# Performance work log

Measured on AMD Instinct MI355X. Metric: run time of the kernel, lower is better.

Reference implementation:

```python
import jax, jax.numpy as jnp
from jax import lax
import numpy as np

D_MODEL = 1024
D_STATE = 16
D_CONV = 4
EXPAND = 2
D_INNER = EXPAND * D_MODEL  # 2048
DT_RANK = D_MODEL // 16     # 64
BATCH = 2
SEQLEN = 1024


def setup_inputs() -> dict:
    key = jax.random.key(0)
    ks = iter(jax.random.split(key, 32))

    def nrm(shape, s=0.02):
        return jax.random.normal(next(ks), shape, jnp.float32) * s

    def mamba_params():
        return dict(
            Win=nrm((2 * D_INNER, D_MODEL)), bin=jnp.zeros((2 * D_INNER,), jnp.float32),
            convw=nrm((D_INNER, D_CONV), 0.1), convb=jnp.zeros((D_INNER,), jnp.float32),
            Wx=nrm((DT_RANK + 2 * D_STATE, D_INNER)),
            Wdt=nrm((D_INNER, DT_RANK), 0.1), bdt=nrm((D_INNER,), 0.1),
            Alog=jnp.log(jnp.broadcast_to(jnp.arange(1, D_STATE + 1, dtype=jnp.float32), (D_INNER, D_STATE))),
            Dsk=jnp.ones((D_INNER,), jnp.float32),
            Wout=nrm((D_MODEL, D_INNER)), bout=jnp.zeros((D_MODEL,), jnp.float32),
        )

    inp = {"x": jax.random.normal(next(ks), (BATCH, SEQLEN, D_MODEL), jnp.float32)}
    for pref, p in (("f_", mamba_params()), ("b_", mamba_params())):
        for k, v in p.items():
            inp[pref + k] = v
    inp["proj_W"] = nrm((D_MODEL, 2 * D_MODEL))
    inp["proj_b"] = jnp.zeros((D_MODEL,), jnp.float32)
    return inp


def selective_scan(u, delta, A, Bm, Cm, Dsk):
    # u, delta: (B,L,Di); Bm, Cm: (B,L,N); A: (Di,N); Dsk: (Di,)
    def step(h, inp):
        u_t, d_t, b_t, c_t = inp  # (B,Di),(B,Di),(B,N),(B,N)
        dA = jnp.exp(d_t[..., None] * A)                      # (B,Di,N)
        h = h * dA + (d_t * u_t)[..., None] * b_t[:, None, :]  # (B,Di,N)
        y = jnp.einsum('bdn,bn->bd', h, c_t)
        return h, y

    h0 = jnp.zeros((u.shape[0], A.shape[0], A.shape[1]), u.dtype)
    xs = (u.transpose(1, 0, 2), delta.transpose(1, 0, 2),
          Bm.transpose(1, 0, 2), Cm.transpose(1, 0, 2))
    _, ys = lax.scan(step, h0, xs)
    return ys.transpose(1, 0, 2) + u * Dsk  # (B,L,Di)


def mamba_fwd(x, Win, bin_, convw, convb, Wx, Wdt, bdt, Alog, Dsk, Wout, bout):
    xz = x @ Win.T + bin_                      # (B,L,2*Di)
    xin, z = jnp.split(xz, 2, axis=-1)
    # causal depthwise conv over time: (B,Di,L)
    xc = lax.conv_general_dilated(
        xin.transpose(0, 2, 1), convw[:, None, :], (1,), [(D_CONV - 1, 0)],
        dimension_numbers=('NCH', 'OIH', 'NCH'), feature_group_count=D_INNER)
    u = jax.nn.silu(xc.transpose(0, 2, 1) + convb)  # (B,L,Di)
    xdbl = u @ Wx.T                                 # (B,L,dt_rank+2N)
    dt, Bm, Cm = jnp.split(xdbl, [DT_RANK, DT_RANK + D_STATE], axis=-1)
    delta = jax.nn.softplus(dt @ Wdt.T + bdt)       # (B,L,Di)
    A = -jnp.exp(Alog)
    y = selective_scan(u, delta, A, Bm, Cm, Dsk)
    y = y * jax.nn.silu(z)
    return y @ Wout.T + bout


def reference(x,
              f_Win, f_bin, f_convw, f_convb, f_Wx, f_Wdt, f_bdt, f_Alog, f_Dsk, f_Wout, f_bout,
              b_Win, b_bin, b_convw, b_convb, b_Wx, b_Wdt, b_bdt, b_Alog, b_Dsk, b_Wout, b_bout,
              proj_W, proj_b):
    out_f = mamba_fwd(x, f_Win, f_bin, f_convw, f_convb, f_Wx, f_Wdt, f_bdt, f_Alog, f_Dsk, f_Wout, f_bout)
    xr = jnp.flip(x, axis=1)
    out_b = mamba_fwd(xr, b_Win, b_bin, b_convw, b_convb, b_Wx, b_Wdt, b_bdt, b_Alog, b_Dsk, b_Wout, b_bout)
    out_b = jnp.flip(out_b, axis=1)
    out = jnp.concatenate([out_f, out_b], axis=-1)  # (B,L,2*d_model)
    return out @ proj_W.T + proj_b
```

## Files before the change

kernel.cpp:

```cpp
#include <hip/hip_runtime.h>
#include <math.h>

#define D_MODEL 1024
#define D_STATE 16
#define D_CONV  4
#define D_INNER 2048
#define DT_RANK 64
#define BATCH   2
#define SEQLEN  1024
#define MROWS   2048
#define XDBL_LD 128
#define NCHUNK  32
#define CLEN    (SEQLEN / NCHUNK)
#define NCHG    8192

typedef __attribute__((ext_vector_type(8))) short bf16x8;
typedef __attribute__((ext_vector_type(4))) float f32x4;

#define BARR() asm volatile("s_barrier" ::: "memory")
#define VMW(n) asm volatile("s_waitcnt vmcnt(" #n ")" ::: "memory")

static __device__ __forceinline__ float sigmoidf_(float x) {
    return 1.f / (1.f + __expf(-x));
}
static __device__ __forceinline__ unsigned short bf16rn(float f) {
    unsigned u = __float_as_uint(f);
    return (unsigned short)((u + 0x7FFFu + ((u >> 16) & 1u)) >> 16);
}
static __device__ __forceinline__ void hl_split(float f, unsigned short& h, unsigned short& l) {
    h = bf16rn(f);
    l = bf16rn(f - __uint_as_float((unsigned)h << 16));
}
static __device__ __forceinline__ float us2f(unsigned short u) {
    return __uint_as_float((unsigned)u << 16);
}

static __device__ __forceinline__
void split_block(const float* __restrict__ in, int R, int C, int ldin,
                 unsigned short* __restrict__ out, int Rout, bool flip,
                 int blk, int tid)
{
    int q = blk * 256 + tid;
    int qpr = C >> 2;
    int row = q / qpr;
    int c4 = (q - row * qpr) << 2;
    if (row >= Rout) return;
    unsigned short h[4] = {0, 0, 0, 0}, l[4] = {0, 0, 0, 0};
    if (row < R) {
        int sr = row;
        if (flip) { int b = row >> 10, t = row & 1023; sr = (b << 10) + (1023 - t); }
        float4 v = *(const float4*)(in + (size_t)sr * ldin + c4);
        float f[4] = {v.x, v.y, v.z, v.w};
        #pragma unroll
        for (int i = 0; i < 4; ++i) hl_split(f[i], h[i], l[i]);
    }
    size_t ob = (size_t)row * (2 * C);
    *(ushort4*)(out + ob + c4)     = make_ushort4(h[0], h[1], h[2], h[3]);
    *(ushort4*)(out + ob + C + c4) = make_ushort4(l[0], l[1], l[2], l[3]);
}

__global__ __launch_bounds__(256)
void prep1_kernel(const float* __restrict__ x,
                  const float* __restrict__ Win0, const float* __restrict__ Win1,
                  const float* __restrict__ Wx0,  const float* __restrict__ Wx1,
                  const float* __restrict__ Wdt0, const float* __restrict__ Wdt1,
                  unsigned short* xc0, unsigned short* xc1,
                  unsigned short* Winb0, unsigned short* Winb1,
                  unsigned short* Wxb0, unsigned short* Wxb1,
                  unsigned short* Wdtb0, unsigned short* Wdtb1)
{
    int b = blockIdx.x, tid = threadIdx.x;
    if      (b < 2048)  split_block(x,    MROWS, D_MODEL, D_MODEL, xc0,  MROWS, false, b,        tid);
    else if (b < 4096)  split_block(x,    MROWS, D_MODEL, D_MODEL, xc1,  MROWS, true,  b - 2048, tid);
    else if (b < 8192)  split_block(Win0, 4096,  D_MODEL, D_MODEL, Winb0, 4096, false, b - 4096, tid);
    else if (b < 12288) split_block(Win1, 4096,  D_MODEL, D_MODEL, Winb1, 4096, false, b - 8192, tid);
    else if (b < 12544) split_block(Wx0,  96,    D_INNER, D_INNER, Wxb0,  128,  false, b - 12288, tid);
    else if (b < 12800) split_block(Wx1,  96,    D_INNER, D_INNER, Wxb1,  128,  false, b - 12544, tid);
    else if (b < 12928) split_block(Wdt0, D_INNER, DT_RANK, DT_RANK, Wdtb0, D_INNER, false, b - 12800, tid);
    else                split_block(Wdt1, D_INNER, DT_RANK, DT_RANK, Wdtb1, D_INNER, false, b - 12928, tid);
}

__global__ __launch_bounds__(256)
void prep2_kernel(const float* __restrict__ Wout0, const float* __restrict__ Wout1,
                  unsigned short* Woutb0, unsigned short* Woutb1)
{
    int b = blockIdx.x, tid = threadIdx.x;
    if (b < 2048) split_block(Wout0, D_MODEL, D_INNER, D_INNER, Woutb0, D_MODEL, false, b, tid);
    else          split_block(Wout1, D_MODEL, D_INNER, D_INNER, Woutb1, D_MODEL, false, b - 2048, tid);
}

#define SWZ(row) (((row) >> 1) & 3)
#define RDA(p, kk, row) (*(const bf16x8*)&AS[p][kk][row][(fs ^ SWZ(row)) << 3])
#define RDB(p, kk, row) (*(const bf16x8*)&BS[p][kk][row][(fs ^ SWZ(row)) << 3])

#define KTILE(MODE, kt) do { \
    const int p_ = (kt) & 1; \
    bf16x8 bF[4]; \
    {  \
        bf16x8 aF[4]; \
        _Pragma("unroll") for (int f = 0; f < 4; ++f) { int rw = wm + f * 16 + fr; aF[f] = RDA(p_, 0, rw); } \
        _Pragma("unroll") for (int g = 0; g < 4; ++g) { int rw = wn + g * 16 + fr; bF[g] = RDB(p_, 0, rw); } \
        if (MODE < 2) stageA((kt) + 1, 1); \
        BARR(); __builtin_amdgcn_s_setprio(1); \
        _Pragma("unroll") for (int f = 0; f < 4; ++f) \
        _Pragma("unroll") for (int g = 0; g < 4; ++g) \
            acc[f][g] = __builtin_amdgcn_mfma_f32_16x16x32_bf16(aF[f], bF[g], acc[f][g], 0, 0, 0); \
        __builtin_amdgcn_s_setprio(0); BARR(); \
    } \
    {  \
        if (MODE == 2) { VMW(0); } else { VMW(8); } \
        bf16x8 aF[4]; \
        _Pragma("unroll") for (int f = 0; f < 4; ++f) { int rw = wm + 64 + f * 16 + fr; aF[f] = RDA(p_, 0, rw); } \
        if (MODE == 0) stageB((kt) + 2, 0); \
        BARR(); __builtin_amdgcn_s_setprio(1); \
        _Pragma("unroll") for (int f = 0; f < 4; ++f) \
        _Pragma("unroll") for (int g = 0; g < 4; ++g) \
            acc[4 + f][g] = __builtin_amdgcn_mfma_f32_16x16x32_bf16(aF[f], bF[g], acc[4 + f][g], 0, 0, 0); \
        __builtin_amdgcn_s_setprio(0); BARR(); \
    } \
    {  \
        bf16x8 aF[4]; \
        _Pragma("unroll") for (int f = 0; f < 4; ++f) { int rw = wm + f * 16 + fr; aF[f] = RDA(p_, 1, rw); } \
        _Pragma("unroll") for (int g = 0; g < 4; ++g) { int rw = wn + g * 16 + fr; bF[g] = RDB(p_, 1, rw); } \
        if (MODE == 0) stageA((kt) + 2, 0); \
        BARR(); __builtin_amdgcn_s_setprio(1); \
        _Pragma("unroll") for (int f = 0; f < 4; ++f) \
        _Pragma("unroll") for (int g = 0; g < 4; ++g) \
            acc[f][g] = __builtin_amdgcn_mfma_f32_16x16x32_bf16(aF[f], bF[g], acc[f][g], 0, 0, 0); \
        __builtin_amdgcn_s_setprio(0); BARR(); \
    } \
    {  \
        if (MODE == 0) { VMW(8); } else if (MODE == 1) { VMW(4); } \
        bf16x8 aF[4]; \
        _Pragma("unroll") for (int f = 0; f < 4; ++f) { int rw = wm + 64 + f * 16 + fr; aF[f] = RDA(p_, 1, rw); } \
        if (MODE == 0) stageB((kt) + 2, 1); \
        BARR(); __builtin_amdgcn_s_setprio(1); \
        _Pragma("unroll") for (int f = 0; f < 4; ++f) \
        _Pragma("unroll") for (int g = 0; g < 4; ++g) \
            acc[4 + f][g] = __builtin_amdgcn_mfma_f32_16x16x32_bf16(aF[f], bF[g], acc[4 + f][g], 0, 0, 0); \
        __builtin_amdgcn_s_setprio(0); BARR(); \
    } \
} while (0)

template<int ACT, bool PART>
__global__ __launch_bounds__(512, 1)
void gemm256(const unsigned short* __restrict__ A0,
             const unsigned short* __restrict__ A1,
             const unsigned short* __restrict__ W0,
             const unsigned short* __restrict__ W1,
             const float* __restrict__ bias0,
             const float* __restrict__ bias1,
             float* __restrict__ C0, float* __restrict__ C1,
             float* __restrict__ part,
             int ldc, int N, int K, int nks, int KTS)
{
    __shared__ unsigned short AS[2][2][256][32];
    __shared__ unsigned short BS[2][2][256][32];

    const int tid = threadIdx.x;
    const int lane = tid & 63;
    const int wid = tid >> 6;

    const int z = blockIdx.z;
    const int dir = z / nks;
    const int ks = z - dir * nks;
    const unsigned short* A = dir ? A1 : A0;
    const unsigned short* W = dir ? W1 : W0;

    const int nbx = gridDim.x;
    const int nwg = nbx * gridDim.y;
    int bid = blockIdx.y * nbx + blockIdx.x;
    int q8 = nwg >> 3;
    int swz = (bid & 7) * q8 + (bid >> 3);
    const int bm = (swz / nbx) * 256;
    const int bn = (swz % nbx) * 256;

    const int ldg = 2 * K;
    const int Kc = KTS * 64;
    const int kbase = ks * Kc;
    const int NT = 3 * KTS;

    const int wm = (wid >> 2) * 128;
    const int wn = (wid & 3) * 64;
    const int fr = lane & 15;
    const int fs = lane >> 4;

    f32x4 acc[8][4];
    #pragma unroll
    for (int i = 0; i < 8; ++i)
        #pragma unroll
        for (int j = 0; j < 4; ++j) {
            f32x4 zv = {0.f, 0.f, 0.f, 0.f};
            acc[i][j] = zv;
        }

    auto koffA = [&](int t) { int sg = t / KTS; int w = t - sg * KTS;
                              return ((sg == 1) ? K : 0) + kbase + w * 64; };
    auto koffB = [&](int t) { int sg = t / KTS; int w = t - sg * KTS;
                              return ((sg == 2) ? K : 0) + kbase + w * 64; };

    auto stageA = [&](int t, int kk) {
        int ko = koffA(t) + kk * 32;
        unsigned short* dst = &AS[t & 1][kk][0][0];
        #pragma unroll
        for (int i = 0; i < 2; ++i) {
            int s = i * 512 + tid;
            int row = s >> 2, sl = s & 3, lsl = sl ^ SWZ(row);
            const unsigned short* src = A + (size_t)(bm + row) * ldg + ko + lsl * 8;
            __builtin_amdgcn_global_load_lds(
                (const __attribute__((address_space(1))) void*)src,
                (__attribute__((address_space(3))) void*)(dst + s * 8), 16, 0, 0);
        }
    };
    auto stageB = [&](int t, int kk) {
        int ko = koffB(t) + kk * 32;
        unsigned short* dst = &BS[t & 1][kk][0][0];
        #pragma unroll
        for (int i = 0; i < 2; ++i) {
            int s = i * 512 + tid;
            int row = s >> 2, sl = s & 3, lsl = sl ^ SWZ(row);
            const unsigned short* src = W + (size_t)(bn + row) * ldg + ko + lsl * 8;
            __builtin_amdgcn_global_load_lds(
                (const __attribute__((address_space(1))) void*)src,
                (__attribute__((address_space(3))) void*)(dst + s * 8), 16, 0, 0);
        }
    };

    stageB(0, 0); stageA(0, 0); stageB(0, 1); stageA(0, 1);
    stageB(1, 0); stageA(1, 0); stageB(1, 1);
    VMW(6);
    BARR();

    for (int kt = 0; kt < NT - 2; ++kt) KTILE(0, kt);
    KTILE(1, NT - 2);
    KTILE(2, NT - 1);

    if (PART) {
        float* P = part + (size_t)z * ((size_t)MROWS * N);
        #pragma unroll
        for (int i = 0; i < 8; ++i)
            #pragma unroll
            for (int j = 0; j < 4; ++j) {
                int coln = bn + wn + j * 16 + fr;
                #pragma unroll
                for (int r = 0; r < 4; ++r) {
                    int rowm = bm + wm + i * 16 + fs * 4 + r;
                    P[(size_t)rowm * N + coln] = acc[i][j][r];
                }
            }
    } else {
        const float* bias = dir ? bias1 : bias0;
        float* C = dir ? C1 : C0;
        #pragma unroll
        for (int i = 0; i < 8; ++i)
            #pragma unroll
            for (int j = 0; j < 4; ++j) {
                int coln = bn + wn + j * 16 + fr;
                float bv = bias ? bias[coln] : 0.f;
                #pragma unroll
                for (int r = 0; r < 4; ++r) {
                    int rowm = bm + wm + i * 16 + fs * 4 + r;
                    float v = acc[i][j][r] + bv;
                    if (ACT == 1) v = (v > 20.f) ? v : log1pf(__expf(v));
                    C[(size_t)rowm * ldc + coln] = v;
                }
            }
    }
}

template<int ACT, bool PART>
__global__ __launch_bounds__(256)
void gemm_mfma(const unsigned short* __restrict__ A0,
               const unsigned short* __restrict__ A1,
               const unsigned short* __restrict__ W0,
               const unsigned short* __restrict__ W1,
               const float* __restrict__ bias0,
               const float* __restrict__ bias1,
               float* __restrict__ C0, float* __restrict__ C1,
               float* __restrict__ part,
               int ldc, int N, int K, int nks)
{
    __shared__ __align__(16) unsigned short As[128 * 32];
    __shared__ __align__(16) unsigned short Bs[128 * 32];

    const int tid = threadIdx.x;
    const int lane = tid & 63;
    const int wid = tid >> 6;

    const int z = blockIdx.z;
    const int dir = z / nks;
    const int ks = z - dir * nks;
    const unsigned short* A = dir ? A1 : A0;
    const unsigned short* W = dir ? W1 : W0;

    const int nbx = gridDim.x;
    const int nwg = nbx * gridDim.y;
    int bid = blockIdx.y * nbx + blockIdx.x;
    int q8 = nwg >> 3;
    int swz = (nwg >= 8) ? (bid & 7) * q8 + (bid >> 3) : bid;
    const int bm = (swz / nbx) * 128;
    const int bn = (swz % nbx) * 128;

    const int ldg = 2 * K;
    const int Kc = K / nks;
    const int kbase = ks * Kc;

    f32x4 acc[4][4];
    #pragma unroll
    for (int i = 0; i < 4; ++i)
        #pragma unroll
        for (int j = 0; j < 4; ++j) {
            f32x4 zv = {0.f, 0.f, 0.f, 0.f};
            acc[i][j] = zv;
        }

    const int r0 = tid >> 2;
    const int k0s = (tid & 3) ^ ((r0 >> 1) & 3);
    const int r1 = (256 + tid) >> 2;
    const int k1s = (tid & 3) ^ ((r1 >> 1) & 3);

    unsigned short* As_w0 = &As[(wid << 6) * 8];
    unsigned short* As_w1 = &As[(256 + (wid << 6)) * 8];
    unsigned short* Bs_w0 = &Bs[(wid << 6) * 8];
    unsigned short* Bs_w1 = &Bs[(256 + (wid << 6)) * 8];

    const int wm = (wid >> 1) * 64;
    const int wn = (wid & 1) * 64;
    const int fr = lane & 15;
    const int fs = lane >> 4;

    const int KS = Kc >> 5;
    #pragma unroll 1
    for (int seg = 0; seg < 3; ++seg) {
        const int aoff = ((seg == 1) ? K : 0) + kbase;
        const int boff = ((seg == 2) ? K : 0) + kbase;
        #pragma unroll 1
        for (int kt = 0; kt < KS; ++kt) {
            const int kk = kt << 5;
            const unsigned short* ga0 = A + (size_t)(bm + r0) * ldg + aoff + kk + k0s * 8;
            const unsigned short* ga1 = A + (size_t)(bm + r1) * ldg + aoff + kk + k1s * 8;
            const unsigned short* gw0 = W + (size_t)(bn + r0) * ldg + boff + kk + k0s * 8;
            const unsigned short* gw1 = W + (size_t)(bn + r1) * ldg + boff + kk + k1s * 8;
            __builtin_amdgcn_global_load_lds(
                (const __attribute__((address_space(1))) void*)ga0,
                (__attribute__((address_space(3))) void*)As_w0, 16, 0, 0);
            __builtin_amdgcn_global_load_lds(
                (const __attribute__((address_space(1))) void*)ga1,
                (__attribute__((address_space(3))) void*)As_w1, 16, 0, 0);
            __builtin_amdgcn_global_load_lds(
                (const __attribute__((address_space(1))) void*)gw0,
                (__attribute__((address_space(3))) void*)Bs_w0, 16, 0, 0);
            __builtin_amdgcn_global_load_lds(
                (const __attribute__((address_space(1))) void*)gw1,
                (__attribute__((address_space(3))) void*)Bs_w1, 16, 0, 0);
            __syncthreads();

            bf16x8 aF[4], bF[4];
            #pragma unroll
            for (int f = 0; f < 4; ++f) {
                int ra = wm + f * 16 + fr;
                int sa = fs ^ ((ra >> 1) & 3);
                aF[f] = *(const bf16x8*)&As[ra * 32 + sa * 8];
                int rb = wn + f * 16 + fr;
                int sb = fs ^ ((rb >> 1) & 3);
                bF[f] = *(const bf16x8*)&Bs[rb * 32 + sb * 8];
            }
            #pragma unroll
            for (int i = 0; i < 4; ++i)
                #pragma unroll
                for (int j = 0; j < 4; ++j)
                    acc[i][j] = __builtin_amdgcn_mfma_f32_16x16x32_bf16(
                        aF[i], bF[j], acc[i][j], 0, 0, 0);
            __syncthreads();
        }
    }

    if (PART) {
        float* P = part + (size_t)z * ((size_t)MROWS * N);
        #pragma unroll
        for (int i = 0; i < 4; ++i)
            #pragma unroll
            for (int j = 0; j < 4; ++j) {
                int coln = bn + wn + j * 16 + fr;
                #pragma unroll
                for (int r = 0; r < 4; ++r) {
                    int rowm = bm + wm + i * 16 + fs * 4 + r;
                    P[(size_t)rowm * N + coln] = acc[i][j][r];
                }
            }
    } else {
        const float* bias = dir ? bias1 : bias0;
        float* C = dir ? C1 : C0;
        #pragma unroll
        for (int i = 0; i < 4; ++i)
            #pragma unroll
            for (int j = 0; j < 4; ++j) {
                int coln = bn + wn + j * 16 + fr;
                float bv = bias ? bias[coln] : 0.f;
                #pragma unroll
                for (int r = 0; r < 4; ++r) {
                    int rowm = bm + wm + i * 16 + fs * 4 + r;
                    float v = acc[i][j][r] + bv;
                    if (ACT == 1) v = (v > 20.f) ? v : log1pf(__expf(v));
                    C[(size_t)rowm * ldc + coln] = v;
                }
            }
    }
}

__global__ __launch_bounds__(256)
void reduce_xdbl_k(const float* __restrict__ part,
                   float* __restrict__ xdbl0, float* __restrict__ xdbl1,
                   unsigned short* __restrict__ dtb0, unsigned short* __restrict__ dtb1)
{
    const int dz = blockIdx.z;
    const float* P = part + (size_t)dz * 16 * MROWS * XDBL_LD;
    float* xdbl = dz ? xdbl1 : xdbl0;
    unsigned short* dtb = dz ? dtb1 : dtb0;
    int i = blockIdx.x * 256 + threadIdx.x;
    int row = i >> 5;
    int c4 = (i & 31) << 2;
    float4 s = make_float4(0.f, 0.f, 0.f, 0.f);
    #pragma unroll
    for (int k = 0; k < 16; ++k) {
        float4 v = *(const float4*)(P + (size_t)k * MROWS * XDBL_LD + (size_t)row * XDBL_LD + c4);
        s.x += v.x; s.y += v.y; s.z += v.z; s.w += v.w;
    }
    *(float4*)(xdbl + (size_t)row * XDBL_LD + c4) = s;
    if (c4 < DT_RANK) {
        float f[4] = {s.x, s.y, s.z, s.w};
        unsigned short h[4], l[4];
        #pragma unroll
        for (int j = 0; j < 4; ++j) hl_split(f[j], h[j], l[j]);
        *(ushort4*)(dtb + (size_t)row * (2 * DT_RANK) + c4) = make_ushort4(h[0], h[1], h[2], h[3]);
        *(ushort4*)(dtb + (size_t)row * (2 * DT_RANK) + DT_RANK + c4) = make_ushort4(l[0], l[1], l[2], l[3]);
    }
}

__global__ __launch_bounds__(256)
void mid_kernel(const float* __restrict__ part2,
                const float* __restrict__ bout0, const float* __restrict__ bout1,
                unsigned short* __restrict__ tmpb,
                const float* __restrict__ projW, unsigned short* __restrict__ pWb)
{
    const int dz = blockIdx.z;
    const int tid = threadIdx.x;
    if (dz == 2) {
        split_block(projW, D_MODEL, 2 * D_MODEL, 2 * D_MODEL, pWb, D_MODEL, false, blockIdx.x, tid);
        return;
    }
    const float* P = part2 + (size_t)dz * 4 * MROWS * D_MODEL;
    const float* bias = dz ? bout1 : bout0;
    const int colofs = dz ? D_MODEL : 0;
    int i = blockIdx.x * 256 + tid;
    int row = i >> 8;
    int c4 = (i & 255) << 2;
    float4 s = make_float4(bias[c4], bias[c4 + 1], bias[c4 + 2], bias[c4 + 3]);
    #pragma unroll
    for (int k = 0; k < 4; ++k) {
        float4 v = *(const float4*)(P + (size_t)k * MROWS * D_MODEL + (size_t)row * D_MODEL + c4);
        s.x += v.x; s.y += v.y; s.z += v.z; s.w += v.w;
    }
    int orow = row;
    if (dz) { int bb = row >> 10, t = row & 1023; orow = (bb << 10) + 1023 - t; }
    float f[4] = {s.x, s.y, s.z, s.w};
    unsigned short h[4], l[4];
    #pragma unroll
    for (int j = 0; j < 4; ++j) hl_split(f[j], h[j], l[j]);
    *(ushort4*)(tmpb + (size_t)orow * 4096 + colofs + c4) = make_ushort4(h[0], h[1], h[2], h[3]);
    *(ushort4*)(tmpb + (size_t)orow * 4096 + 2048 + colofs + c4) = make_ushort4(l[0], l[1], l[2], l[3]);
}

__global__ __launch_bounds__(256)
void reduce_out_k(const float* __restrict__ part, const float* __restrict__ bias,
                  float* __restrict__ out)
{
    int i = blockIdx.x * 256 + threadIdx.x;
    int row = i >> 8;
    int c4 = (i & 255) << 2;
    float4 s = make_float4(bias[c4], bias[c4 + 1], bias[c4 + 2], bias[c4 + 3]);
    #pragma unroll
    for (int k = 0; k < 8; ++k) {
        float4 v = *(const float4*)(part + (size_t)k * MROWS * D_MODEL + (size_t)row * D_MODEL + c4);
        s.x += v.x; s.y += v.y; s.z += v.z; s.w += v.w;
    }
    *(float4*)(out + (size_t)row * D_MODEL + c4) = s;
}

__global__ __launch_bounds__(256)
void conv_silu_kernel(const float* __restrict__ xz0, const float* __restrict__ xz1,
                      const float* __restrict__ cw0, const float* __restrict__ cw1,
                      const float* __restrict__ cb0, const float* __restrict__ cb1,
                      unsigned short* __restrict__ ub0, unsigned short* __restrict__ ub1)
{
    const int dz = blockIdx.z;
    const float* xz = dz ? xz1 : xz0;
    const float* convw = dz ? cw1 : cw0;
    const float* convb = dz ? cb1 : cb0;
    unsigned short* ub = dz ? ub1 : ub0;
    int idx = blockIdx.x * 256 + threadIdx.x;
    int d = idx % D_INNER;
    int r = idx / D_INNER;
    int t = r % SEQLEN;
    float acc = convb[d];
    #pragma unroll
    for (int k = 0; k < D_CONV; ++k) {
        int back = D_CONV - 1 - k;
        if (t - back >= 0)
            acc += xz[(size_t)(r - back) * (2 * D_INNER) + d] * convw[d * D_CONV + k];
    }
    float v = acc * sigmoidf_(acc);
    unsigned short h, l;
    hl_split(v, h, l);
    ub[(size_t)r * (2 * D_INNER) + d] = h;
    ub[(size_t)r * (2 * D_INNER) + D_INNER + d] = l;
}

__global__ __launch_bounds__(256)
void scan_phase1(const float* __restrict__ delta0, const float* __restrict__ delta1,
                 const unsigned short* __restrict__ ub0, const unsigned short* __restrict__ ub1,
                 const float* __restrict__ xdbl0, const float* __restrict__ xdbl1,
                 const float* __restrict__ Alog0, const float* __restrict__ Alog1,
                 float* __restrict__ aprod, float* __restrict__ hfin)
{
    const int gid = blockIdx.x * 256 + threadIdx.x;
    const int chg = gid & (NCHG - 1);
    const int chunk = gid >> 13;
    const int dir = chg >> 12;
    const int bd = chg & 4095;
    const int b = bd >> 11, d = bd & 2047;
    const float* delta = dir ? delta1 : delta0;
    const unsigned short* ub = dir ? ub1 : ub0;
    const float* xdbl = dir ? xdbl1 : xdbl0;
    const float* Alog = dir ? Alog1 : Alog0;

    float Av[16], h[16], ap[16];
    #pragma unroll
    for (int n = 0; n < 16; ++n) {
        Av[n] = -__expf(Alog[d * D_STATE + n]);
        h[n] = 0.f; ap[n] = 1.f;
    }
    const int t0 = chunk * CLEN;
    for (int t = t0; t < t0 + CLEN; ++t) {
        const size_t r = (size_t)b * SEQLEN + t;
        float dlt = delta[r * D_INNER + d];
        float uu = us2f(ub[r * 4096 + d]) + us2f(ub[r * 4096 + 2048 + d]);
        float du = dlt * uu;
        float4 bq[4];
        #pragma unroll
        for (int q = 0; q < 4; ++q)
            bq[q] = *(const float4*)(xdbl + r * XDBL_LD + DT_RANK + q * 4);
        #pragma unroll
        for (int n = 0; n < 16; ++n) {
            float Bv = ((const float*)&bq[n >> 2])[n & 3];
            float dA = __expf(dlt * Av[n]);
            h[n] = h[n] * dA + du * Bv;
            ap[n] *= dA;
        }
    }
    float* pa = aprod + (size_t)chunk * (NCHG * 16) + (size_t)chg * 16;
    float* pf = hfin  + (size_t)chunk * (NCHG * 16) + (size_t)chg * 16;
    #pragma unroll
    for (int q = 0; q < 4; ++q) {
        *(float4*)(pa + q * 4) = make_float4(ap[q*4], ap[q*4+1], ap[q*4+2], ap[q*4+3]);
        *(float4*)(pf + q * 4) = make_float4(h[q*4], h[q*4+1], h[q*4+2], h[q*4+3]);
    }
}

__global__ __launch_bounds__(256)
void scan_phase2(float* __restrict__ aprod ,
                 const float* __restrict__ hfin)
{
    const int gid = blockIdx.x * 256 + threadIdx.x;
    float h = 0.f;
    for (int c = 0; c < NCHUNK; ++c) {
        const size_t idx = (size_t)c * (NCHG * 16) + gid;
        float a = aprod[idx];
        float f = hfin[idx];
        aprod[idx] = h;
        h = a * h + f;
    }
}

__global__ __launch_bounds__(256)
void scan_phase3(const float* __restrict__ delta0, const float* __restrict__ delta1,
                 unsigned short* __restrict__ ub0, unsigned short* __restrict__ ub1,
                 const float* __restrict__ xdbl0, const float* __restrict__ xdbl1,
                 const float* __restrict__ Alog0, const float* __restrict__ Alog1,
                 const float* __restrict__ Dsk0, const float* __restrict__ Dsk1,
                 const float* __restrict__ xz0, const float* __restrict__ xz1,
                 const float* __restrict__ hin)
{
    const int gid = blockIdx.x * 256 + threadIdx.x;
    const int chg = gid & (NCHG - 1);
    const int chunk = gid >> 13;
    const int dir = chg >> 12;
    const int bd = chg & 4095;
    const int b = bd >> 11, d = bd & 2047;
    const float* delta = dir ? delta1 : delta0;
    unsigned short* ub = dir ? ub1 : ub0;
    const float* xdbl = dir ? xdbl1 : xdbl0;
    const float* Alog = dir ? Alog1 : Alog0;
    const float* Dsk = dir ? Dsk1 : Dsk0;
    const float* xz = dir ? xz1 : xz0;

    float Av[16], h[16];
    const float* ph = hin + (size_t)chunk * (NCHG * 16) + (size_t)chg * 16;
    #pragma unroll
    for (int n = 0; n < 16; ++n) {
        Av[n] = -__expf(Alog[d * D_STATE + n]);
        h[n] = ph[n];
    }
    const float Dv = Dsk[d];
    const int t0 = chunk * CLEN;
    for (int t = t0; t < t0 + CLEN; ++t) {
        const size_t r = (size_t)b * SEQLEN + t;
        float dlt = delta[r * D_INNER + d];
        float uu = us2f(ub[r * 4096 + d]) + us2f(ub[r * 4096 + 2048 + d]);
        float du = dlt * uu;
        float4 bq[4], cq[4];
        #pragma unroll
        for (int q = 0; q < 4; ++q) {
            bq[q] = *(const float4*)(xdbl + r * XDBL_LD + DT_RANK + q * 4);
            cq[q] = *(const float4*)(xdbl + r * XDBL_LD + DT_RANK + D_STATE + q * 4);
        }
        float p0 = 0.f, p1 = 0.f, p2 = 0.f, p3 = 0.f;
        #pragma unroll
        for (int n = 0; n < 16; ++n) {
            float Bv = ((const float*)&bq[n >> 2])[n & 3];
            float Cv = ((const float*)&cq[n >> 2])[n & 3];
            float dA = __expf(dlt * Av[n]);
            h[n] = h[n] * dA + du * Bv;
            if ((n & 3) == 0) p0 += h[n] * Cv;
            else if ((n & 3) == 1) p1 += h[n] * Cv;
            else if ((n & 3) == 2) p2 += h[n] * Cv;
            else p3 += h[n] * Cv;
        }
        float y = ((p0 + p1) + (p2 + p3)) + uu * Dv;
        float zv = xz[r * (2 * D_INNER) + D_INNER + d];
        float v = y * (zv * sigmoidf_(zv));
        unsigned short hh, ll;
        hl_split(v, hh, ll);
        ub[r * 4096 + d] = hh;
        ub[r * 4096 + 2048 + d] = ll;
    }
}

extern "C" void kernel_launch(void* const* d_in, const int* in_sizes, int n_in,
                              void* d_out, int out_size, void* d_ws, size_t ws_size,
                              hipStream_t stream)
{
    const float* x = (const float*)d_in[0];
    const float* proj_W = (const float*)d_in[23];
    const float* proj_b = (const float*)d_in[24];
    float* out = (float*)d_out;

    const float *Win[2], *bin_[2], *convw[2], *convb[2], *Wx[2], *Wdt[2], *bdt[2],
                *Alog[2], *Dsk[2], *Wout[2], *bout[2];
    for (int dir = 0; dir < 2; ++dir) {
        const int base = 1 + dir * 11;
        Win[dir]   = (const float*)d_in[base + 0];
        bin_[dir]  = (const float*)d_in[base + 1];
        convw[dir] = (const float*)d_in[base + 2];
        convb[dir] = (const float*)d_in[base + 3];
        Wx[dir]    = (const float*)d_in[base + 4];
        Wdt[dir]   = (const float*)d_in[base + 5];
        bdt[dir]   = (const float*)d_in[base + 6];
        Alog[dir]  = (const float*)d_in[base + 7];
        Dsk[dir]   = (const float*)d_in[base + 8];
        Wout[dir]  = (const float*)d_in[base + 9];
        bout[dir]  = (const float*)d_in[base + 10];
    }

    char* ws = (char*)d_ws;
    const size_t MB = 1ull << 20;
    float* xz[2]            = {(float*)(ws + 0 * MB),   (float*)(ws + 32 * MB)};
    unsigned short* ub[2]   = {(unsigned short*)(ws + 64 * MB),
                               (unsigned short*)(ws + 80 * MB)};
    unsigned short* Winb[2] = {(unsigned short*)(ws + 96 * MB),
                               (unsigned short*)(ws + 112 * MB)};
    unsigned short* xc[2]   = {(unsigned short*)(ws + 128 * MB),
                               (unsigned short*)(ws + 136 * MB)};
    float* part             = (float*)(ws + 112 * MB);
    float* part2            = (float*)(ws + 0 * MB);
    float* delta[2]         = {(float*)(ws + 112 * MB), (float*)(ws + 128 * MB)};
    unsigned short* Woutb[2]= {(unsigned short*)(ws + 96 * MB),
                               (unsigned short*)(ws + 104 * MB)};
    unsigned short* yzb[2]  = {ub[0], ub[1]};
    unsigned short* tmpb    = ub[0];
    unsigned short* pWb     = ub[1];
    unsigned short* Wxb[2]  = {(unsigned short*)(ws + 144 * MB), (unsigned short*)(ws + 145 * MB)};
    unsigned short* Wdtb[2] = {(unsigned short*)(ws + 146 * MB), (unsigned short*)(ws + 146 * MB + 512 * 1024)};
    unsigned short* dtb[2]  = {(unsigned short*)(ws + 147 * MB), (unsigned short*)(ws + 147 * MB + 512 * 1024)};
    float* xdbl[2]          = {(float*)(ws + 148 * MB), (float*)(ws + 149 * MB)};
    float* aprod            = (float*)(ws + 150 * MB);
    float* hfin             = (float*)(ws + 167 * MB);

    dim3 blk(256);

    prep1_kernel<<<13056, blk, 0, stream>>>(
        x, Win[0], Win[1], Wx[0], Wx[1], Wdt[0], Wdt[1],
        xc[0], xc[1], Winb[0], Winb[1], Wxb[0], Wxb[1], Wdtb[0], Wdtb[1]);

    gemm256<0, false><<<dim3(16, 8, 2), dim3(512), 0, stream>>>(
        xc[0], xc[1], Winb[0], Winb[1], bin_[0], bin_[1], xz[0], xz[1],
        nullptr, 4096, 4096, D_MODEL, 1, 16);

    prep2_kernel<<<4096, blk, 0, stream>>>(Wout[0], Wout[1], Woutb[0], Woutb[1]);

    conv_silu_kernel<<<dim3((MROWS * D_INNER) / 256, 1, 2), blk, 0, stream>>>(
        xz[0], xz[1], convw[0], convw[1], convb[0], convb[1], ub[0], ub[1]);

    gemm_mfma<0, true><<<dim3(1, 16, 32), blk, 0, stream>>>(
        ub[0], ub[1], Wxb[0], Wxb[1], nullptr, nullptr, nullptr, nullptr,
        part, XDBL_LD, XDBL_LD, D_INNER, 16);

    reduce_xdbl_k<<<dim3(256, 1, 2), blk, 0, stream>>>(
        part, xdbl[0], xdbl[1], dtb[0], dtb[1]);

    gemm_mfma<1, false><<<dim3(16, 16, 2), blk, 0, stream>>>(
        dtb[0], dtb[1], Wdtb[0], Wdtb[1], bdt[0], bdt[1], delta[0], delta[1],
        nullptr, D_INNER, D_INNER, DT_RANK, 1);

    scan_phase1<<<NCHUNK * NCHG / 256, blk, 0, stream>>>(
        delta[0], delta[1], ub[0], ub[1], xdbl[0], xdbl[1], Alog[0], Alog[1],
        aprod, hfin);
    scan_phase2<<<NCHG * 16 / 256, blk, 0, stream>>>(aprod, hfin);
    scan_phase3<<<NCHUNK * NCHG / 256, blk, 0, stream>>>(
        delta[0], delta[1], ub[0], ub[1], xdbl[0], xdbl[1], Alog[0], Alog[1],
        Dsk[0], Dsk[1], xz[0], xz[1], aprod);

    gemm256<0, true><<<dim3(4, 8, 8), dim3(512), 0, stream>>>(
        yzb[0], yzb[1], Woutb[0], Woutb[1], nullptr, nullptr, nullptr, nullptr,
        part2, D_MODEL, D_MODEL, D_INNER, 4, 8);

    mid_kernel<<<dim3(2048, 1, 3), blk, 0, stream>>>(
        part2, bout[0], bout[1], tmpb, proj_W, pWb);

    gemm256<0, true><<<dim3(4, 8, 8), dim3(512), 0, stream>>>(
        tmpb, nullptr, pWb, nullptr, nullptr, nullptr, nullptr, nullptr,
        part2, D_MODEL, D_MODEL, 2 * D_MODEL, 8, 4);

    reduce_out_k<<<2048, blk, 0, stream>>>(part2, proj_b, out);
}
```

Before: 491.4 us.

## Share unflipped input across directions and fold Wout split into conv kernel

The in-projection GEMM now runs once over the unflipped bf16-split input with the two directions' weights concatenated along N. The backward half flips rows at store time, which removes the separate flipped copy of x and its split pass. The Wout hi/lo split moves from its own kernel into an extra grid slice of the conv/SiLU kernel, saving a launch. KTS becomes a template parameter so the k-offset division is resolved at compile time, and the main K loop is marked not to unroll. The risk is scattered row writes in the flipped epilogue and a heavier combined conv kernel.

After: 482.3 us. No clear change (-1.9%).

```diff
diff --git a/kernel.cpp b/kernel.cpp
--- a/kernel.cpp
+++ b/kernel.cpp
@@ -64,29 +64,19 @@
                   const float* __restrict__ Win0, const float* __restrict__ Win1,
                   const float* __restrict__ Wx0,  const float* __restrict__ Wx1,
                   const float* __restrict__ Wdt0, const float* __restrict__ Wdt1,
-                  unsigned short* xc0, unsigned short* xc1,
+                  unsigned short* xc0,
                   unsigned short* Winb0, unsigned short* Winb1,
                   unsigned short* Wxb0, unsigned short* Wxb1,
                   unsigned short* Wdtb0, unsigned short* Wdtb1)
 {
     int b = blockIdx.x, tid = threadIdx.x;
     if      (b < 2048)  split_block(x,    MROWS, D_MODEL, D_MODEL, xc0,  MROWS, false, b,        tid);
-    else if (b < 4096)  split_block(x,    MROWS, D_MODEL, D_MODEL, xc1,  MROWS, true,  b - 2048, tid);
-    else if (b < 8192)  split_block(Win0, 4096,  D_MODEL, D_MODEL, Winb0, 4096, false, b - 4096, tid);
-    else if (b < 12288) split_block(Win1, 4096,  D_MODEL, D_MODEL, Winb1, 4096, false, b - 8192, tid);
-    else if (b < 12544) split_block(Wx0,  96,    D_INNER, D_INNER, Wxb0,  128,  false, b - 12288, tid);
-    else if (b < 12800) split_block(Wx1,  96,    D_INNER, D_INNER, Wxb1,  128,  false, b - 12544, tid);
-    else if (b < 12928) split_block(Wdt0, D_INNER, DT_RANK, DT_RANK, Wdtb0, D_INNER, false, b - 12800, tid);
-    else                split_block(Wdt1, D_INNER, DT_RANK, DT_RANK, Wdtb1, D_INNER, false, b - 12928, tid);
-}
-
-__global__ __launch_bounds__(256)
-void prep2_kernel(const float* __restrict__ Wout0, const float* __restrict__ Wout1,
-                  unsigned short* Woutb0, unsigned short* Woutb1)
-{
-    int b = blockIdx.x, tid = threadIdx.x;
-    if (b < 2048) split_block(Wout0, D_MODEL, D_INNER, D_INNER, Woutb0, D_MODEL, false, b, tid);
-    else          split_block(Wout1, D_MODEL, D_INNER, D_INNER, Woutb1, D_MODEL, false, b - 2048, tid);
+    else if (b < 6144)  split_block(Win0, 4096,  D_MODEL, D_MODEL, Winb0, 4096, false, b - 2048, tid);
+    else if (b < 10240) split_block(Win1, 4096,  D_MODEL, D_MODEL, Winb1, 4096, false, b - 6144, tid);
+    else if (b < 10496) split_block(Wx0,  96,    D_INNER, D_INNER, Wxb0,  128,  false, b - 10240, tid);
+    else if (b < 10752) split_block(Wx1,  96,    D_INNER, D_INNER, Wxb1,  128,  false, b - 10496, tid);
+    else if (b < 10880) split_block(Wdt0, D_INNER, DT_RANK, DT_RANK, Wdtb0, D_INNER, false, b - 10752, tid);
+    else                split_block(Wdt1, D_INNER, DT_RANK, DT_RANK, Wdtb1, D_INNER, false, b - 10880, tid);
 }
 
 #define SWZ(row) (((row) >> 1) & 3)
@@ -142,7 +132,7 @@
     } \
 } while (0)
 
-template<int ACT, bool PART>
+template<int ACT, bool PART, int KTS, bool DUALN>
 __global__ __launch_bounds__(512, 1)
 void gemm256(const unsigned short* __restrict__ A0,
              const unsigned short* __restrict__ A1,
@@ -152,7 +142,7 @@
              const float* __restrict__ bias1,
              float* __restrict__ C0, float* __restrict__ C1,
              float* __restrict__ part,
-             int ldc, int N, int K, int nks, int KTS)
+             int ldc, int N, int K, int nks)
 {
     __shared__ unsigned short AS[2][2][256][32];
     __shared__ unsigned short BS[2][2][256][32];
@@ -162,10 +152,8 @@
     const int wid = tid >> 6;
 
     const int z = blockIdx.z;
-    const int dir = z / nks;
-    const int ks = z - dir * nks;
-    const unsigned short* A = dir ? A1 : A0;
-    const unsigned short* W = dir ? W1 : W0;
+    const int zdir = z / nks;
+    const int ks = z - zdir * nks;
 
     const int nbx = gridDim.x;
     const int nwg = nbx * gridDim.y;
@@ -175,10 +163,16 @@
     const int bm = (swz / nbx) * 256;
     const int bn = (swz % nbx) * 256;
 
+    int dn, bnn;
+    if (DUALN) { dn = (bn >= (N >> 1)) ? 1 : 0; bnn = bn - dn * (N >> 1); }
+    else       { dn = zdir; bnn = bn; }
+    const unsigned short* A = (DUALN || dn == 0) ? A0 : A1;
+    const unsigned short* W = dn ? W1 : W0;
+
     const int ldg = 2 * K;
+    constexpr int NT = 3 * KTS;
     const int Kc = KTS * 64;
     const int kbase = ks * Kc;
-    const int NT = 3 * KTS;
 
     const int wm = (wid >> 2) * 128;
     const int wn = (wid & 3) * 64;
@@ -194,10 +188,12 @@
             acc[i][j] = zv;
         }
 
-    auto koffA = [&](int t) { int sg = t / KTS; int w = t - sg * KTS;
-                              return ((sg == 1) ? K : 0) + kbase + w * 64; };
-    auto koffB = [&](int t) { int sg = t / KTS; int w = t - sg * KTS;
-                              return ((sg == 2) ? K : 0) + kbase + w * 64; };
+    auto koffA = [&](int t) { unsigned tu = (unsigned)t; unsigned sg = tu / KTS;
+                              unsigned w = tu - sg * KTS;
+                              return (int)((sg == 1 ? (unsigned)K : 0u) + kbase + w * 64); };
+    auto koffB = [&](int t) { unsigned tu = (unsigned)t; unsigned sg = tu / KTS;
+                              unsigned w = tu - sg * KTS;
+                              return (int)((sg == 2 ? (unsigned)K : 0u) + kbase + w * 64); };
 
     auto stageA = [&](int t, int kk) {
         int ko = koffA(t) + kk * 32;
@@ -219,7 +215,7 @@
         for (int i = 0; i < 2; ++i) {
             int s = i * 512 + tid;
             int row = s >> 2, sl = s & 3, lsl = sl ^ SWZ(row);
-            const unsigned short* src = W + (size_t)(bn + row) * ldg + ko + lsl * 8;
+            const unsigned short* src = W + (size_t)(bnn + row) * ldg + ko + lsl * 8;
             __builtin_amdgcn_global_load_lds(
                 (const __attribute__((address_space(1))) void*)src,
                 (__attribute__((address_space(3))) void*)(dst + s * 8), 16, 0, 0);
@@ -231,6 +227,7 @@
     VMW(6);
     BARR();
 
+    #pragma unroll 1
     for (int kt = 0; kt < NT - 2; ++kt) KTILE(0, kt);
     KTILE(1, NT - 2);
     KTILE(2, NT - 1);
@@ -241,7 +238,7 @@
         for (int i = 0; i < 8; ++i)
             #pragma unroll
             for (int j = 0; j < 4; ++j) {
-                int coln = bn + wn + j * 16 + fr;
+                int coln = bnn + wn + j * 16 + fr;
                 #pragma unroll
                 for (int r = 0; r < 4; ++r) {
                     int rowm = bm + wm + i * 16 + fs * 4 + r;
@@ -249,20 +246,22 @@
                 }
             }
     } else {
-        const float* bias = dir ? bias1 : bias0;
-        float* C = dir ? C1 : C0;
+        const float* bias = dn ? bias1 : bias0;
+        float* C = dn ? C1 : C0;
         #pragma unroll
         for (int i = 0; i < 8; ++i)
             #pragma unroll
             for (int j = 0; j < 4; ++j) {
-                int coln = bn + wn + j * 16 + fr;
+                int coln = bnn + wn + j * 16 + fr;
                 float bv = bias ? bias[coln] : 0.f;
                 #pragma unroll
                 for (int r = 0; r < 4; ++r) {
                     int rowm = bm + wm + i * 16 + fs * 4 + r;
                     float v = acc[i][j][r] + bv;
                     if (ACT == 1) v = (v > 20.f) ? v : log1pf(__expf(v));
-                    C[(size_t)rowm * ldc + coln] = v;
+                    int crow = rowm;
+                    if (DUALN && dn) { int bb = rowm >> 10, t = rowm & 1023; crow = (bb << 10) + 1023 - t; }
+                    C[(size_t)crow * ldc + coln] = v;
                 }
             }
     }
@@ -488,17 +487,26 @@
 }
 
 __global__ __launch_bounds__(256)
-void conv_silu_kernel(const float* __restrict__ xz0, const float* __restrict__ xz1,
+void conv_prep_kernel(const float* __restrict__ xz0, const float* __restrict__ xz1,
                       const float* __restrict__ cw0, const float* __restrict__ cw1,
                       const float* __restrict__ cb0, const float* __restrict__ cb1,
-                      unsigned short* __restrict__ ub0, unsigned short* __restrict__ ub1)
+                      unsigned short* __restrict__ ub0, unsigned short* __restrict__ ub1,
+                      const float* __restrict__ Wout0, const float* __restrict__ Wout1,
+                      unsigned short* __restrict__ Woutb0, unsigned short* __restrict__ Woutb1)
 {
     const int dz = blockIdx.z;
+    const int tid = threadIdx.x;
+    if (dz == 2) {
+        int b = blockIdx.x;
+        if (b < 2048) split_block(Wout0, D_MODEL, D_INNER, D_INNER, Woutb0, D_MODEL, false, b, tid);
+        else if (b < 4096) split_block(Wout1, D_MODEL, D_INNER, D_INNER, Woutb1, D_MODEL, false, b - 2048, tid);
+        return;
+    }
     const float* xz = dz ? xz1 : xz0;
     const float* convw = dz ? cw1 : cw0;
     const float* convb = dz ? cb1 : cb0;
     unsigned short* ub = dz ? ub1 : ub0;
-    int idx = blockIdx.x * 256 + threadIdx.x;
+    int idx = blockIdx.x * 256 + tid;
     int d = idx % D_INNER;
     int r = idx / D_INNER;
     int t = r % SEQLEN;
@@ -679,8 +687,7 @@
                                (unsigned short*)(ws + 80 * MB)};
     unsigned short* Winb[2] = {(unsigned short*)(ws + 96 * MB),
                                (unsigned short*)(ws + 112 * MB)};
-    unsigned short* xc[2]   = {(unsigned short*)(ws + 128 * MB),
-                               (unsigned short*)(ws + 136 * MB)};
+    unsigned short* xc0     = (unsigned short*)(ws + 128 * MB);
     float* part             = (float*)(ws + 112 * MB);
     float* part2            = (float*)(ws + 0 * MB);
     float* delta[2]         = {(float*)(ws + 112 * MB), (float*)(ws + 128 * MB)};
@@ -698,18 +705,17 @@
 
     dim3 blk(256);
 
-    prep1_kernel<<<13056, blk, 0, stream>>>(
+    prep1_kernel<<<11008, blk, 0, stream>>>(
         x, Win[0], Win[1], Wx[0], Wx[1], Wdt[0], Wdt[1],
-        xc[0], xc[1], Winb[0], Winb[1], Wxb[0], Wxb[1], Wdtb[0], Wdtb[1]);
-
-    gemm256<0, false><<<dim3(16, 8, 2), dim3(512), 0, stream>>>(
-        xc[0], xc[1], Winb[0], Winb[1], bin_[0], bin_[1], xz[0], xz[1],
-        nullptr, 4096, 4096, D_MODEL, 1, 16);
-
-    prep2_kernel<<<4096, blk, 0, stream>>>(Wout[0], Wout[1], Woutb[0], Woutb[1]);
-
-    conv_silu_kernel<<<dim3((MROWS * D_INNER) / 256, 1, 2), blk, 0, stream>>>(
-        xz[0], xz[1], convw[0], convw[1], convb[0], convb[1], ub[0], ub[1]);
+        xc0, Winb[0], Winb[1], Wxb[0], Wxb[1], Wdtb[0], Wdtb[1]);
+
+    gemm256<0, false, 16, true><<<dim3(32, 8, 1), dim3(512), 0, stream>>>(
+        xc0, nullptr, Winb[0], Winb[1], bin_[0], bin_[1], xz[0], xz[1],
+        nullptr, 4096, 8192, D_MODEL, 1);
+
+    conv_prep_kernel<<<dim3((MROWS * D_INNER) / 256, 1, 3), blk, 0, stream>>>(
+        xz[0], xz[1], convw[0], convw[1], convb[0], convb[1], ub[0], ub[1],
+        Wout[0], Wout[1], Woutb[0], Woutb[1]);
 
     gemm_mfma<0, true><<<dim3(1, 16, 32), blk, 0, stream>>>(
         ub[0], ub[1], Wxb[0], Wxb[1], nullptr, nullptr, nullptr, nullptr,
@@ -730,16 +736,16 @@
         delta[0], delta[1], ub[0], ub[1], xdbl[0], xdbl[1], Alog[0], Alog[1],
         Dsk[0], Dsk[1], xz[0], xz[1], aprod);
 
-    gemm256<0, true><<<dim3(4, 8, 8), dim3(512), 0, stream>>>(
+    gemm256<0, true, 8, false><<<dim3(4, 8, 8), dim3(512), 0, stream>>>(
         yzb[0], yzb[1], Woutb[0], Woutb[1], nullptr, nullptr, nullptr, nullptr,
-        part2, D_MODEL, D_MODEL, D_INNER, 4, 8);
+        part2, D_MODEL, D_MODEL, D_INNER, 4);
 
     mid_kernel<<<dim3(2048, 1, 3), blk, 0, stream>>>(
         part2, bout[0], bout[1], tmpb, proj_W, pWb);
 
-    gemm256<0, true><<<dim3(4, 8, 8), dim3(512), 0, stream>>>(
+    gemm256<0, true, 4, false><<<dim3(4, 8, 8), dim3(512), 0, stream>>>(
         tmpb, nullptr, pWb, nullptr, nullptr, nullptr, nullptr, nullptr,
-        part2, D_MODEL, D_MODEL, 2 * D_MODEL, 8, 4);
+        part2, D_MODEL, D_MODEL, 2 * D_MODEL, 8);
 
     reduce_out_k<<<2048, blk, 0, stream>>>(part2, proj_b, out);
 }
```
